# Optimization experiments

Hardware: AMD Instinct MI355X
Metric: run time of the kernel (lower is better)

The kernel has to match this reference:

```python
import jax, jax.numpy as jnp
import numpy as np
import math

BS, S, D = 2, 2048, 2048
DOWN, UP, H, RD = 512, 1024, 16, 32
HD = D // H            # 128, used only in softmax scale
VD = UP // H           # 64 per-head value dim
CD = UP // H           # 64 per-head content q/k dim
SCALE = math.sqrt(HD) + math.sqrt(RD)


def _rope(x, head_dim):
    # x: [bs, heads, seq, head_dim]; standard rotate-half RoPE
    seq = x.shape[2]
    inv_freq = 1.0 / (10000.0 ** (jnp.arange(0, head_dim, 2, dtype=jnp.float32) / head_dim))
    freqs = jnp.arange(seq, dtype=jnp.float32)[:, None] * inv_freq[None, :]  # [S, hd/2]
    emb = jnp.concatenate([freqs, freqs], axis=-1)                            # [S, hd]
    cos = jnp.cos(emb)[None, None]
    sin = jnp.sin(emb)[None, None]
    x1, x2 = x[..., : head_dim // 2], x[..., head_dim // 2 :]
    rot = jnp.concatenate([-x2, x1], axis=-1)
    return x * cos + rot * sin


def setup_inputs() -> dict:
    key = jax.random.key(0)
    ks = jax.random.split(key, 10)
    sd = 0.02
    inp = {
        'h': jax.random.normal(ks[0], (BS, S, D), jnp.float32),
        'mask': jnp.tril(jnp.ones((1, 1, S, S), jnp.int32)),
        'Wdkv': jax.random.normal(ks[1], (DOWN, D), jnp.float32) * sd,
        'bdkv': jnp.zeros((DOWN,), jnp.float32),
        'Wuk': jax.random.normal(ks[2], (UP, DOWN), jnp.float32) * sd,
        'buk': jnp.zeros((UP,), jnp.float32),
        'Wuv': jax.random.normal(ks[3], (UP, DOWN), jnp.float32) * sd,
        'buv': jnp.zeros((UP,), jnp.float32),
        'Wdq': jax.random.normal(ks[4], (DOWN, D), jnp.float32) * sd,
        'bdq': jnp.zeros((DOWN,), jnp.float32),
        'Wuq': jax.random.normal(ks[5], (UP, DOWN), jnp.float32) * sd,
        'buq': jnp.zeros((UP,), jnp.float32),
        'Wqr': jax.random.normal(ks[6], (RD * H, DOWN), jnp.float32) * sd,
        'bqr': jnp.zeros((RD * H,), jnp.float32),
        'Wkr': jax.random.normal(ks[7], (RD, D), jnp.float32) * sd,
        'bkr': jnp.zeros((RD,), jnp.float32),
        'Wfc': jax.random.normal(ks[8], (D, H * VD), jnp.float32) * sd,
        'bfc': jnp.zeros((D,), jnp.float32),
    }
    return inp


def reference(h, mask, Wdkv, bdkv, Wuk, buk, Wuv, buv, Wdq, bdq, Wuq, buq,
              Wqr, bqr, Wkr, bkr, Wfc, bfc):
    bs, seq, _ = h.shape
    # low-rank KV path
    c_kv = h @ Wdkv.T + bdkv                                   # [bs,S,DOWN]
    k_c = (c_kv @ Wuk.T + buk).reshape(bs, seq, H, CD).transpose(0, 2, 1, 3)
    v_c = (c_kv @ Wuv.T + buv).reshape(bs, seq, H, VD).transpose(0, 2, 1, 3)
    # low-rank Q path
    c_q = h @ Wdq.T + bdq                                      # [bs,S,DOWN]
    q_c = (c_q @ Wuq.T + buq).reshape(bs, seq, H, CD).transpose(0, 2, 1, 3)
    # decoupled RoPE paths
    q_r = _rope((c_q @ Wqr.T + bqr).reshape(bs, seq, H, RD).transpose(0, 2, 1, 3), RD)
    k_r = _rope((h @ Wkr.T + bkr).reshape(bs, seq, 1, RD).transpose(0, 2, 1, 3), RD)
    k_r = jnp.broadcast_to(k_r, (bs, H, seq, RD))              # shared RoPE key across heads
    q = jnp.concatenate([q_c, q_r], axis=-1)                   # [bs,H,S,CD+RD]
    k = jnp.concatenate([k_c, k_r], axis=-1)
    scores = jnp.einsum('bhqd,bhkd->bhqk', q, k)
    # NB: original applies mask BEFORE dividing by scale
    scores = jnp.where(mask == 0, -1e9, scores)
    probs = jax.nn.softmax(scores / SCALE, axis=-1)
    out = jnp.einsum('bhqk,bhkd->bhqd', probs, v_c)            # [bs,H,S,VD]
    out = out.transpose(0, 2, 1, 3).reshape(bs, seq, H * VD)
    return out @ Wfc.T + bfc
```

## Files before the change

kernel.cpp:

```cpp
#include <hip/hip_runtime.h>
#include <hip/hip_bf16.h>
#include <math.h>

typedef unsigned short u16;
typedef __attribute__((ext_vector_type(8))) short bf16x8;
typedef __attribute__((ext_vector_type(4))) float f32x4;
typedef __attribute__((ext_vector_type(16))) float f32x16;

namespace {

constexpr int BS = 2;
constexpr int S = 2048;
constexpr int D = 2048;
constexpr int DOWN = 512;
constexpr int UP = 1024;
constexpr int H = 16;
constexpr int RD = 32;
constexpr int VD = 64;
constexpr int QKD = 96;
constexpr int M = BS * S;
constexpr int N1 = 1152;
constexpr int N2 = 2048;
constexpr int N3 = 1536;
constexpr long PACK_V8 = (long)BS * H * S * QKD / 8;

__device__ __forceinline__ float b2f(u16 u) {
  unsigned int x = ((unsigned int)u) << 16;
  return __uint_as_float(x);
}
__device__ __forceinline__ u16 f2b(float f) {
  unsigned int u = __float_as_uint(f);
  u += 0x7fff + ((u >> 16) & 1);
  return (u16)(u >> 16);
}
__device__ __forceinline__ void store_out(float* p, float v) { *p = v; }
__device__ __forceinline__ void store_out(u16* p, float v) { *p = f2b(v); }

__device__ __forceinline__ void async16(const u16* g, u16* lds) {
  __builtin_amdgcn_global_load_lds(
      (const __attribute__((address_space(1))) unsigned int*)g,
      (__attribute__((address_space(3))) unsigned int*)lds, 16, 0, 0);
}

__device__ __forceinline__ float exp2_fast(float x) {
#if __has_builtin(__builtin_amdgcn_exp2f)
  return __builtin_amdgcn_exp2f(x);
#else
  float r;
  asm("v_exp_f32 %0, %1" : "=v"(r) : "v"(x));
  return r;
#endif
}

__device__ __forceinline__ unsigned pkbf(float a, float b) {
  union { __hip_bfloat162 h; unsigned u; } c;
  c.h = __float22bfloat162_rn(make_float2(a, b));
  return c.u;
}
__device__ __forceinline__ void plswap(unsigned& a, unsigned& b) {
  asm("v_permlane32_swap_b32 %0, %1" : "+v"(a), "+v"(b));
}

__device__ __forceinline__ f32x4 mfma32(bf16x8 a, bf16x8 b, f32x4 c) {
  return __builtin_amdgcn_mfma_f32_16x16x32_bf16(a, b, c, 0, 0, 0);
}
__device__ __forceinline__ f32x16 mfma3216(bf16x8 a, bf16x8 b, f32x16 c) {
  return __builtin_amdgcn_mfma_f32_32x32x16_bf16(a, b, c, 0, 0, 0);
}

__global__ __launch_bounds__(256) void prep_kernel(
    const float* __restrict__ h, const float* __restrict__ Wdkv,
    const float* __restrict__ Wdq, const float* __restrict__ Wkr,
    const float* __restrict__ Wuk, const float* __restrict__ Wuv,
    const float* __restrict__ Wuq, const float* __restrict__ Wqr,
    const float* __restrict__ Wfc, const float* __restrict__ bdkv,
    const float* __restrict__ bdq, const float* __restrict__ bkr,
    const float* __restrict__ buk, const float* __restrict__ buv,
    const float* __restrict__ buq, const float* __restrict__ bqr,
    u16* __restrict__ hb, u16* __restrict__ Wcat1, u16* __restrict__ Wcat2,
    u16* __restrict__ Wcat3, u16* __restrict__ Wfcb,
    float* __restrict__ bcat1, float* __restrict__ bcat2,
    float* __restrict__ bcat3, float* __restrict__ ct, float* __restrict__ st) {
  const long i = (long)blockIdx.x * 256 + threadIdx.x;
  if (i >= 3630240) return;
  if (i < 3620864) {
    const float* src; u16* dst; long off;
    if      (i < 2097152) { src = h;    dst = hb;              off = i; }
    else if (i < 2359296) { src = Wdkv; dst = Wcat1;           off = i - 2097152; }
    else if (i < 2621440) { src = Wdq;  dst = Wcat1 + 1048576; off = i - 2359296; }
    else if (i < 2637824) { src = Wkr;  dst = Wcat1 + 2097152; off = i - 2621440; }
    else if (i < 2768896) { src = Wuk;  dst = Wcat2;           off = i - 2637824; }
    else if (i < 2899968) { src = Wuv;  dst = Wcat2 + 524288;  off = i - 2768896; }
    else if (i < 3031040) { src = Wuq;  dst = Wcat3;           off = i - 2899968; }
    else if (i < 3096576) { src = Wqr;  dst = Wcat3 + 524288;  off = i - 3031040; }
    else                  { src = Wfc;  dst = Wfcb;            off = i - 3096576; }
    float4 v = ((const float4*)src)[off];
    ushort4 o;
    o.x = f2b(v.x); o.y = f2b(v.y); o.z = f2b(v.z); o.w = f2b(v.w);
    ((ushort4*)dst)[off] = o;
  } else if (i < 3622048) {
    long j0 = (i - 3620864) * 4;
#pragma unroll
    for (int e = 0; e < 4; ++e) {
      long j = j0 + e;
      if (j < N1) {
        float v = 0.f;
        if (j < 512) v = bdkv[j];
        else if (j < 1024) v = bdq[j - 512];
        else if (j < 1056) v = bkr[j - 1024];
        bcat1[j] = v;
      } else if (j < N1 + N2) {
        long jj = j - N1;
        bcat2[jj] = (jj < 1024) ? buk[jj] : buv[jj - 1024];
      } else {
        long jj = j - N1 - N2;
        bcat3[jj] = (jj < 1024) ? buq[jj] : bqr[jj - 1024];
      }
    }
  } else {
    long k0 = (i - 3622048) * 4;
#pragma unroll
    for (int e = 0; e < 4; ++e) {
      long k = k0 + e;
      int s = (int)(k >> 4), r = (int)(k & 15);
      float f = powf(10000.f, -(float)r / 16.f);
      float th = (float)s * f;
      ct[k] = cosf(th);
      st[k] = sinf(th);
    }
  }
}

template <int BM, int BN, typename OutT>
__device__ __forceinline__ void gemm_body(
    const u16* __restrict__ A, int lda, const u16* __restrict__ W, int ldw,
    const float* __restrict__ bias, OutT* __restrict__ C, int ldc, int K,
    int m0, int n0) {
  constexpr int MW = BM / 32;
  constexpr int NW = BN / 32;
  constexpr int AI = BM / 16;
  constexpr int TI = AI + BN / 16;
  __shared__ u16 As[2][BM * 32];
  __shared__ u16 Bs[2][BN * 32];
  const int t = threadIdx.x;
  const int lane = t & 63, wave = t >> 6;
  const int wm = (wave >> 1) * (BM / 2), wn = (wave & 1) * (BN / 2);
  const int lrow = lane & 15, lk = (lane >> 4) * 8;
  const int srow = lane >> 2, scol = (lane & 3) * 8;
  f32x4 acc[MW][NW] = {};

  auto stage = [&](int buf, int k0) {
    for (int i = wave; i < TI; i += 4) {
      if (i < AI) {
        int r = i * 16 + srow;
        async16(A + (size_t)(m0 + r) * lda + k0 + scol, &As[buf][i * 512]);
      } else {
        int r = (i - AI) * 16 + srow;
        async16(W + (size_t)(n0 + r) * ldw + k0 + scol,
                &Bs[buf][(i - AI) * 512]);
      }
    }
  };

  const int nt = K / 32;
  stage(0, 0);
  __syncthreads();
  for (int ti = 0; ti < nt; ++ti) {
    const int buf = ti & 1;
    if (ti + 1 < nt) stage(buf ^ 1, (ti + 1) * 32);
    bf16x8 af[MW], bfr[NW];
#pragma unroll
    for (int i = 0; i < MW; ++i)
      af[i] = *(const bf16x8*)(&As[buf][(wm + i * 16 + lrow) * 32 + lk]);
#pragma unroll
    for (int i = 0; i < NW; ++i)
      bfr[i] = *(const bf16x8*)(&Bs[buf][(wn + i * 16 + lrow) * 32 + lk]);
#pragma unroll
    for (int mi = 0; mi < MW; ++mi)
#pragma unroll
      for (int ni = 0; ni < NW; ++ni)
        acc[mi][ni] = mfma32(af[mi], bfr[ni], acc[mi][ni]);
    __syncthreads();
  }
#pragma unroll
  for (int mi = 0; mi < MW; ++mi)
#pragma unroll
    for (int ni = 0; ni < NW; ++ni)
#pragma unroll
      for (int r = 0; r < 4; ++r) {
        int m = m0 + wm + mi * 16 + (lane >> 4) * 4 + r;
        int n = n0 + wn + ni * 16 + lrow;
        store_out(C + (size_t)m * ldc + n, acc[mi][ni][r] + bias[n]);
      }
}

template <int BM, int BN, typename OutT>
__global__ __launch_bounds__(256) void gemm_bt_mfma(
    const u16* __restrict__ A, int lda, const u16* __restrict__ W, int ldw,
    const float* __restrict__ bias, OutT* __restrict__ C, int ldc, int K) {
  gemm_body<BM, BN, OutT>(A, lda, W, ldw, bias, C, ldc, K,
                          blockIdx.x * BM, blockIdx.y * BN);
}

__global__ __launch_bounds__(256) void gemm_up_fused(
    const u16* __restrict__ C1v, const u16* __restrict__ Wcat2,
    const u16* __restrict__ Wcat3, const float* __restrict__ bcat2,
    const float* __restrict__ bcat3, u16* __restrict__ C2,
    u16* __restrict__ C3) {
  const int by = blockIdx.y;
  const u16* A;
  const u16* W;
  const float* bias;
  u16* C;
  int ldc, n0;
  if (by < 16) {
    A = C1v; W = Wcat2; bias = bcat2; C = C2; ldc = N2; n0 = by * 128;
  } else {
    A = C1v + DOWN; W = Wcat3; bias = bcat3; C = C3; ldc = N3;
    n0 = (by - 16) * 128;
  }
  gemm_body<128, 128, u16>(A, N1, W, DOWN, bias, C, ldc, DOWN,
                           blockIdx.x * 128, n0);
}

__global__ __launch_bounds__(256) void reshape_kernel(
    const u16* __restrict__ qc, const u16* __restrict__ qr,
    const u16* __restrict__ kc,
    const u16* __restrict__ kr,
    const float* __restrict__ ct, const float* __restrict__ st,
    const u16* __restrict__ vin,
    u16* __restrict__ Qp, u16* __restrict__ Kp, u16* __restrict__ VtB) {
  const int bid = blockIdx.x;
  if (bid < 6144) {
    const long i = (long)bid * 256 + threadIdx.x;
    const int which = (i >= PACK_V8);
    const long j8 = which ? i - PACK_V8 : i;
    const int g = (int)(j8 % 12);
    const long row = j8 / 12;
    const int s = (int)(row & (S - 1));
    const int h = (int)((row >> 11) & 15);
    const int b = (int)(row >> 15);
    bf16x8 o;
    if (which == 0) {
      const float sc = 1.44269504088896f / (sqrtf(128.f) + sqrtf(32.f));
      if (g < 8) {
        bf16x8 v =
            *(const bf16x8*)(qc + (size_t)(b * S + s) * N3 + h * VD + g * 8);
#pragma unroll
        for (int e = 0; e < 8; ++e) o[e] = (short)f2b(b2f((u16)v[e]) * sc);
      } else {
        const int r0 = (g - 8) * 8;
        const u16* qrow = qr + (size_t)(b * S + s) * N3 + h * RD;
        bf16x8 x8 = *(const bf16x8*)(qrow + r0);
        bf16x8 xp8 = *(const bf16x8*)(qrow + (r0 ^ 16));
        const float* cb = ct + s * 16 + (r0 & 15);
        const float* sn = st + s * 16 + (r0 & 15);
        const float sg = (r0 < 16) ? -1.f : 1.f;
#pragma unroll
        for (int e = 0; e < 8; ++e) {
          float val = b2f((u16)x8[e]) * cb[e] + sg * b2f((u16)xp8[e]) * sn[e];
          o[e] = (short)f2b(val * sc);
        }
      }
      *(bf16x8*)(Qp + j8 * 8) = o;
    } else {
      if (g < 8) {
        o = *(const bf16x8*)(kc + (size_t)(b * S + s) * N2 + h * VD + g * 8);
      } else {
        const int r0 = (g - 8) * 8;
        const u16* krow = kr + (size_t)(b * S + s) * N1;
        bf16x8 x8 = *(const bf16x8*)(krow + r0);
        bf16x8 xp8 = *(const bf16x8*)(krow + (r0 ^ 16));
        const float* cb = ct + s * 16 + (r0 & 15);
        const float* sn = st + s * 16 + (r0 & 15);
        const float sg = (r0 < 16) ? -1.f : 1.f;
#pragma unroll
        for (int e = 0; e < 8; ++e) {
          float val = b2f((u16)x8[e]) * cb[e] + sg * b2f((u16)xp8[e]) * sn[e];
          o[e] = (short)f2b(val);
        }
      }
      *(bf16x8*)(Kp + j8 * 8) = o;
    }
  } else {
    __shared__ u16 tile[64][72];
    const int tb = bid - 6144;
    const int m0 = (tb & 63) * 64;
    const int h = tb >> 6;
    const int r = threadIdx.x >> 2, c0 = (threadIdx.x & 3) * 16;
    *(bf16x8*)(&tile[r][c0]) =
        *(const bf16x8*)(vin + (size_t)(m0 + r) * N2 + h * VD + c0);
    *(bf16x8*)(&tile[r][c0 + 8]) =
        *(const bf16x8*)(vin + (size_t)(m0 + r) * N2 + h * VD + c0 + 8);
    __syncthreads();
    bf16x8 o0, o1;
#pragma unroll
    for (int jj = 0; jj < 8; ++jj) {
      o0[jj] = (short)tile[c0 + jj][r];
      o1[jj] = (short)tile[c0 + 8 + jj][r];
    }
    const int b = m0 / S, sb = m0 % S;
    size_t dst = ((size_t)(b * H + h) * 64 + ((sb + c0) >> 5)) * 2048 +
                 (size_t)r * 32 + ((sb + c0) & 31);
    *(bf16x8*)(VtB + dst) = o0;
    *(bf16x8*)(VtB + dst + 8) = o1;
  }
}

__global__ __launch_bounds__(256, 3) void attn_mfma(
    const u16* __restrict__ Qp, const u16* __restrict__ Kp,
    const u16* __restrict__ Vt, u16* __restrict__ attnb) {
  const int t = threadIdx.x, wave = t >> 6, lane = t & 63;
  const int l31 = lane & 31, hw = lane >> 5;
  const int xcd = (int)(blockIdx.x & 7), sub = (int)(blockIdx.x >> 3);
  const int bh = xcd * 4 + (sub & 3);
  const int tile = 63 - (sub >> 2);
  const int b = bh >> 4, h = bh & 15;
  const int q0w = tile * 32;
  const size_t hbo = (size_t)bh * S;
  constexpr long KSTR = (long)4 * 32 * QKD;
  constexpr long VSTR = (long)4 * 2048;

  __shared__ float red[3][64][33];

  bf16x8 qf[6];
  {
    const u16* qrow = Qp + (hbo + q0w + l31) * QKD + hw * 8;
#pragma unroll
    for (int c = 0; c < 6; ++c) qf[c] = *(const bf16x8*)(qrow + c * 16);
  }
  const f32x16 ZERO16 = {0,0,0,0,0,0,0,0,0,0,0,0,0,0,0,0};
  f32x16 O0 = ZERO16, O1 = ZERO16;
  float lsum = 0.f;
  const int q_abs = q0w + l31;
  const u16* vptr = Vt + (size_t)bh * 64 * 2048 + l31 * 32 + 8 * hw +
                    (size_t)wave * 2048;
  const u16* kptr = Kp + (hbo + (size_t)(wave * 32 + l31)) * QKD + hw * 8;

  auto loadK = [&](bf16x8* kf) {
#pragma unroll
    for (int c = 0; c < 6; ++c) kf[c] = *(const bf16x8*)(kptr + c * 16);
  };
  auto loadV = [&](const u16* p, bf16x8* vf) {
    vf[0] = *(const bf16x8*)(p);
    vf[1] = *(const bf16x8*)(p + 16);
    vf[2] = *(const bf16x8*)(p + 1024);
    vf[3] = *(const bf16x8*)(p + 1040);
  };
  auto finish = [&](const f32x16& sa, const f32x16& sb, const bf16x8* vf,
                    int m) {
    float e[16];
    if (m == tile) {
      const int k0 = m * 32;
#pragma unroll
      for (int r = 0; r < 16; ++r) {
        int key_abs = k0 + (r & 3) + 8 * (r >> 2) + 4 * hw;
        float v = exp2_fast(sa[r] + sb[r]);
        e[r] = (key_abs <= q_abs) ? v : 0.f;
      }
    } else {
#pragma unroll
      for (int r = 0; r < 16; ++r) e[r] = exp2_fast(sa[r] + sb[r]);
    }
    {
      float p0 = (e[0] + e[1]) + (e[2] + e[3]);
      float p1 = (e[4] + e[5]) + (e[6] + e[7]);
      float p2 = (e[8] + e[9]) + (e[10] + e[11]);
      float p3 = (e[12] + e[13]) + (e[14] + e[15]);
      lsum += (p0 + p1) + (p2 + p3);
    }
    unsigned w0 = pkbf(e[0], e[1]),   w1 = pkbf(e[2], e[3]);
    unsigned w2 = pkbf(e[4], e[5]),   w3 = pkbf(e[6], e[7]);
    unsigned w4 = pkbf(e[8], e[9]),   w5 = pkbf(e[10], e[11]);
    unsigned w6 = pkbf(e[12], e[13]), w7 = pkbf(e[14], e[15]);
    plswap(w0, w2); plswap(w1, w3); plswap(w4, w6); plswap(w5, w7);
    union { unsigned u[4]; bf16x8 v; } ua, ub;
    ua.u[0] = w0; ua.u[1] = w1; ua.u[2] = w2; ua.u[3] = w3;
    ub.u[0] = w4; ub.u[1] = w5; ub.u[2] = w6; ub.u[3] = w7;
    __builtin_amdgcn_s_setprio(1);
    O0 = mfma3216(ua.v, vf[0], O0);
    O1 = mfma3216(ua.v, vf[2], O1);
    O0 = mfma3216(ub.v, vf[1], O0);
    O1 = mfma3216(ub.v, vf[3], O1);
    __builtin_amdgcn_s_setprio(0);
  };

  if (tile >= wave) {
    bf16x8 kf[6], vfE[4], vfO[4];
    loadK(kf);
    loadV(vptr, vfE);
    int m = wave;
    while (true) {
      {
        const bool pf = (m + 4 <= tile);
        if (pf) { vptr += VSTR; loadV(vptr, vfO); }
        __builtin_amdgcn_s_setprio(1);
        f32x16 sa = mfma3216(kf[0], qf[0], ZERO16);
        f32x16 sb = mfma3216(kf[1], qf[1], ZERO16);
        sa = mfma3216(kf[2], qf[2], sa);
        sb = mfma3216(kf[3], qf[3], sb);
        sa = mfma3216(kf[4], qf[4], sa);
        sb = mfma3216(kf[5], qf[5], sb);
        __builtin_amdgcn_s_setprio(0);
        if (pf) { kptr += KSTR; loadK(kf); }
        finish(sa, sb, vfE, m);
      }
      m += 4;
      if (m > tile) break;
      {
        const bool pf = (m + 4 <= tile);
        if (pf) { vptr += VSTR; loadV(vptr, vfE); }
        __builtin_amdgcn_s_setprio(1);
        f32x16 sa = mfma3216(kf[0], qf[0], ZERO16);
        f32x16 sb = mfma3216(kf[1], qf[1], ZERO16);
        sa = mfma3216(kf[2], qf[2], sa);
        sb = mfma3216(kf[3], qf[3], sb);
        sa = mfma3216(kf[4], qf[4], sa);
        sb = mfma3216(kf[5], qf[5], sb);
        __builtin_amdgcn_s_setprio(0);
        if (pf) { kptr += KSTR; loadK(kf); }
        finish(sa, sb, vfO, m);
      }
      m += 4;
      if (m > tile) break;
    }
  }

  if (wave > 0) {
#pragma unroll
    for (int r = 0; r < 16; ++r) {
      red[wave - 1][lane][r] = O0[r];
      red[wave - 1][lane][16 + r] = O1[r];
    }
    red[wave - 1][lane][32] = lsum;
  }
  __syncthreads();
  if (wave == 0) {
#pragma unroll
    for (int w = 0; w < 3; ++w) {
#pragma unroll
      for (int r = 0; r < 16; ++r) {
        O0[r] += red[w][lane][r];
        O1[r] += red[w][lane][16 + r];
      }
      lsum += red[w][lane][32];
    }
    float tot = lsum + __shfl_xor(lsum, 32);
    u16* ob = attnb + (size_t)b * S * UP + h * VD;
#pragma unroll
    for (int r = 0; r < 16; ++r) {
      int rowq = (r & 3) + 8 * (r >> 2) + 4 * hw;
      float linv = 1.f / __shfl(tot, rowq);
      size_t rowoff = (size_t)(q0w + rowq) * UP;
      ob[rowoff + l31] = f2b(O0[r] * linv);
      ob[rowoff + 32 + l31] = f2b(O1[r] * linv);
    }
  }
}

}

extern "C" void kernel_launch(void* const* d_in, const int* in_sizes, int n_in,
                              void* d_out, int out_size, void* d_ws, size_t ws_size,
                              hipStream_t stream) {
  const float* h    = (const float*)d_in[0];
  const float* Wdkv = (const float*)d_in[2];
  const float* bdkv = (const float*)d_in[3];
  const float* Wuk  = (const float*)d_in[4];
  const float* buk  = (const float*)d_in[5];
  const float* Wuv  = (const float*)d_in[6];
  const float* buv  = (const float*)d_in[7];
  const float* Wdq  = (const float*)d_in[8];
  const float* bdq  = (const float*)d_in[9];
  const float* Wuq  = (const float*)d_in[10];
  const float* buq  = (const float*)d_in[11];
  const float* Wqr  = (const float*)d_in[12];
  const float* bqr  = (const float*)d_in[13];
  const float* Wkr  = (const float*)d_in[14];
  const float* bkr  = (const float*)d_in[15];
  const float* Wfc  = (const float*)d_in[16];
  const float* bfc  = (const float*)d_in[17];
  float* out = (float*)d_out;

  u16* p = (u16*)d_ws;
  u16* hb    = p; p += (size_t)M * D;
  u16* Wcat1 = p; p += (size_t)N1 * D;
  u16* Wcat2 = p; p += (size_t)N2 * DOWN;
  u16* Wcat3 = p; p += (size_t)N3 * DOWN;
  u16* Wfcb  = p; p += (size_t)D * UP;
  u16* C1    = p; p += (size_t)M * N1;
  u16* C2    = p; p += (size_t)M * N2;
  u16* C3    = p; p += (size_t)M * N3;
  u16* Qp    = p; p += 6291456;
  u16* Kp    = p; p += 6291456;
  u16* Vt    = p; p += (size_t)UP * M;
  float* bcat1 = (float*)p; p += 2 * N1;
  float* bcat2 = (float*)p; p += 2 * N2;
  float* bcat3 = (float*)p; p += 2 * N3;
  float* ct = (float*)p; p += 2 * S * 16;
  float* st = (float*)p; p += 2 * S * 16;
  u16* attnb = C1;

  prep_kernel<<<dim3(14181), 256, 0, stream>>>(
      h, Wdkv, Wdq, Wkr, Wuk, Wuv, Wuq, Wqr, Wfc,
      bdkv, bdq, bkr, buk, buv, buq, bqr,
      hb, Wcat1, Wcat2, Wcat3, Wfcb, bcat1, bcat2, bcat3, ct, st);

  gemm_bt_mfma<64, 64, u16><<<dim3(M / 64, N1 / 64), 256, 0, stream>>>(
      hb, D, Wcat1, D, bcat1, C1, N1, D);
  gemm_up_fused<<<dim3(M / 128, 28), 256, 0, stream>>>(
      C1, Wcat2, Wcat3, bcat2, bcat3, C2, C3);

  reshape_kernel<<<dim3(7168), 256, 0, stream>>>(
      C3, C3 + UP, C2, C1 + 2 * DOWN, ct, st, C2 + UP, Qp, Kp, Vt);

  attn_mfma<<<dim3(2048), 256, 0, stream>>>(Qp, Kp, Vt, attnb);

  gemm_bt_mfma<64, 128, float><<<dim3(M / 64, D / 128), 256, 0, stream>>>(
      attnb, UP, Wfcb, UP, bfc, out, D, UP);
}
```

Baseline: 304.4 us.

## Fuse Q/K content packing into up-projection epilogue and fold softmax scale into weights

```diff
diff --git a/kernel.cpp b/kernel.cpp
--- a/kernel.cpp
+++ b/kernel.cpp
@@ -22,7 +22,7 @@
 constexpr int N1 = 1152;
 constexpr int N2 = 2048;
 constexpr int N3 = 1536;
-constexpr long PACK_V8 = (long)BS * H * S * QKD / 8;
+constexpr long ROPE_V8 = (long)BS * H * S * 4;
 
 __device__ __forceinline__ float b2f(u16 u) {
   unsigned int x = ((unsigned int)u) << 16;
@@ -83,20 +83,22 @@
     float* __restrict__ bcat3, float* __restrict__ ct, float* __restrict__ st) {
   const long i = (long)blockIdx.x * 256 + threadIdx.x;
   if (i >= 3630240) return;
+  const float SC = 1.44269504088896f / (sqrtf(128.f) + sqrtf(32.f));
   if (i < 3620864) {
-    const float* src; u16* dst; long off;
+    const float* src; u16* dst; long off; float scl = 1.f;
     if      (i < 2097152) { src = h;    dst = hb;              off = i; }
     else if (i < 2359296) { src = Wdkv; dst = Wcat1;           off = i - 2097152; }
     else if (i < 2621440) { src = Wdq;  dst = Wcat1 + 1048576; off = i - 2359296; }
     else if (i < 2637824) { src = Wkr;  dst = Wcat1 + 2097152; off = i - 2621440; }
     else if (i < 2768896) { src = Wuk;  dst = Wcat2;           off = i - 2637824; }
     else if (i < 2899968) { src = Wuv;  dst = Wcat2 + 524288;  off = i - 2768896; }
-    else if (i < 3031040) { src = Wuq;  dst = Wcat3;           off = i - 2899968; }
-    else if (i < 3096576) { src = Wqr;  dst = Wcat3 + 524288;  off = i - 3031040; }
+    else if (i < 3031040) { src = Wuq;  dst = Wcat3;           off = i - 2899968; scl = SC; }
+    else if (i < 3096576) { src = Wqr;  dst = Wcat3 + 524288;  off = i - 3031040; scl = SC; }
     else                  { src = Wfc;  dst = Wfcb;            off = i - 3096576; }
     float4 v = ((const float4*)src)[off];
     ushort4 o;
-    o.x = f2b(v.x); o.y = f2b(v.y); o.z = f2b(v.z); o.w = f2b(v.w);
+    o.x = f2b(v.x * scl); o.y = f2b(v.y * scl);
+    o.z = f2b(v.z * scl); o.w = f2b(v.w * scl);
     ((ushort4*)dst)[off] = o;
   } else if (i < 3622048) {
     long j0 = (i - 3620864) * 4;
@@ -114,7 +116,7 @@
         bcat2[jj] = (jj < 1024) ? buk[jj] : buv[jj - 1024];
       } else {
         long jj = j - N1 - N2;
-        bcat3[jj] = (jj < 1024) ? buq[jj] : bqr[jj - 1024];
+        bcat3[jj] = ((jj < 1024) ? buq[jj] : bqr[jj - 1024]) * SC;
       }
     }
   } else {
@@ -132,10 +134,63 @@
 }
 
 template <int BM, int BN, typename OutT>
-__device__ __forceinline__ void gemm_body(
+__device__ __forceinline__ void gemm_body_sb(
     const u16* __restrict__ A, int lda, const u16* __restrict__ W, int ldw,
     const float* __restrict__ bias, OutT* __restrict__ C, int ldc, int K,
     int m0, int n0) {
+  constexpr int MW = BM / 32;
+  constexpr int NW = BN / 32;
+  constexpr int AI = BM / 16;
+  constexpr int TI = AI + BN / 16;
+  __shared__ u16 As[BM * 32];
+  __shared__ u16 Bs[BN * 32];
+  const int t = threadIdx.x;
+  const int lane = t & 63, wave = t >> 6;
+  const int wm = (wave >> 1) * (BM / 2), wn = (wave & 1) * (BN / 2);
+  const int lrow = lane & 15, lk = (lane >> 4) * 8;
+  const int srow = lane >> 2, scol = (lane & 3) * 8;
+  f32x4 acc[MW][NW] = {};
+  for (int k0 = 0; k0 < K; k0 += 32) {
+    __syncthreads();
+    for (int i = wave; i < TI; i += 4) {
+      if (i < AI) {
+        int r = i * 16 + srow;
+        async16(A + (size_t)(m0 + r) * lda + k0 + scol, As + i * 512);
+      } else {
+        int r = (i - AI) * 16 + srow;
+        async16(W + (size_t)(n0 + r) * ldw + k0 + scol, Bs + (i - AI) * 512);
+      }
+    }
+    __syncthreads();
+    bf16x8 af[MW], bfr[NW];
+#pragma unroll
+    for (int i = 0; i < MW; ++i)
+      af[i] = *(const bf16x8*)(As + (wm + i * 16 + lrow) * 32 + lk);
+#pragma unroll
+    for (int i = 0; i < NW; ++i)
+      bfr[i] = *(const bf16x8*)(Bs + (wn + i * 16 + lrow) * 32 + lk);
+#pragma unroll
+    for (int mi = 0; mi < MW; ++mi)
+#pragma unroll
+      for (int ni = 0; ni < NW; ++ni)
+        acc[mi][ni] = mfma32(af[mi], bfr[ni], acc[mi][ni]);
+  }
+#pragma unroll
+  for (int mi = 0; mi < MW; ++mi)
+#pragma unroll
+    for (int ni = 0; ni < NW; ++ni)
+#pragma unroll
+      for (int r = 0; r < 4; ++r) {
+        int m = m0 + wm + mi * 16 + (lane >> 4) * 4 + r;
+        int n = n0 + wn + ni * 16 + lrow;
+        store_out(C + (size_t)m * ldc + n, acc[mi][ni][r] + bias[n]);
+      }
+}
+
+template <int BM, int BN, typename F>
+__device__ __forceinline__ void gemm_core_db(
+    const u16* __restrict__ A, int lda, const u16* __restrict__ W, int ldw,
+    const float* __restrict__ bias, int K, int m0, int n0, F&& emit) {
   constexpr int MW = BM / 32;
   constexpr int NW = BN / 32;
   constexpr int AI = BM / 16;
@@ -190,101 +245,104 @@
       for (int r = 0; r < 4; ++r) {
         int m = m0 + wm + mi * 16 + (lane >> 4) * 4 + r;
         int n = n0 + wn + ni * 16 + lrow;
-        store_out(C + (size_t)m * ldc + n, acc[mi][ni][r] + bias[n]);
+        emit(m, n, acc[mi][ni][r] + bias[n]);
       }
 }
 
 template <int BM, int BN, typename OutT>
-__global__ __launch_bounds__(256) void gemm_bt_mfma(
+__global__ __launch_bounds__(256) void gemm_bt_sb(
     const u16* __restrict__ A, int lda, const u16* __restrict__ W, int ldw,
     const float* __restrict__ bias, OutT* __restrict__ C, int ldc, int K) {
-  gemm_body<BM, BN, OutT>(A, lda, W, ldw, bias, C, ldc, K,
-                          blockIdx.x * BM, blockIdx.y * BN);
+  gemm_body_sb<BM, BN, OutT>(A, lda, W, ldw, bias, C, ldc, K,
+                             blockIdx.x * BM, blockIdx.y * BN);
+}
+
+template <int BM, int BN, typename OutT>
+__global__ __launch_bounds__(256) void gemm_bt_db(
+    const u16* __restrict__ A, int lda, const u16* __restrict__ W, int ldw,
+    const float* __restrict__ bias, OutT* __restrict__ C, int ldc, int K) {
+  gemm_core_db<BM, BN>(A, lda, W, ldw, bias, K, blockIdx.x * BM,
+                       blockIdx.y * BN, [&](int m, int n, float v) {
+                         store_out(C + (size_t)m * ldc + n, v);
+                       });
 }
 
 __global__ __launch_bounds__(256) void gemm_up_fused(
     const u16* __restrict__ C1v, const u16* __restrict__ Wcat2,
     const u16* __restrict__ Wcat3, const float* __restrict__ bcat2,
     const float* __restrict__ bcat3, u16* __restrict__ C2,
-    u16* __restrict__ C3) {
+    u16* __restrict__ C3, u16* __restrict__ Qp, u16* __restrict__ Kp) {
   const int by = blockIdx.y;
-  const u16* A;
-  const u16* W;
-  const float* bias;
-  u16* C;
-  int ldc, n0;
   if (by < 16) {
-    A = C1v; W = Wcat2; bias = bcat2; C = C2; ldc = N2; n0 = by * 128;
+    gemm_core_db<128, 128>(
+        C1v, N1, Wcat2, DOWN, bcat2, DOWN, blockIdx.x * 128, by * 128,
+        [&](int m, int n, float v) {
+          if (n < 1024) {
+            int b = m >> 11, s = m & 2047, hh = n >> 6, d = n & 63;
+            Kp[((size_t)(b * 16 + hh) * 2048 + s) * 96 + d] = f2b(v);
+          } else {
+            C2[(size_t)m * N2 + n] = f2b(v);
+          }
+        });
   } else {
-    A = C1v + DOWN; W = Wcat3; bias = bcat3; C = C3; ldc = N3;
-    n0 = (by - 16) * 128;
-  }
-  gemm_body<128, 128, u16>(A, N1, W, DOWN, bias, C, ldc, DOWN,
-                           blockIdx.x * 128, n0);
+    gemm_core_db<128, 128>(
+        C1v + DOWN, N1, Wcat3, DOWN, bcat3, DOWN, blockIdx.x * 128,
+        (by - 16) * 128, [&](int m, int n, float v) {
+          if (n < 1024) {
+            int b = m >> 11, s = m & 2047, hh = n >> 6, d = n & 63;
+            Qp[((size_t)(b * 16 + hh) * 2048 + s) * 96 + d] = f2b(v);
+          } else {
+            C3[(size_t)m * N3 + n] = f2b(v);
+          }
+        });
+  }
 }
 
 __global__ __launch_bounds__(256) void reshape_kernel(
-    const u16* __restrict__ qc, const u16* __restrict__ qr,
-    const u16* __restrict__ kc,
+    const u16* __restrict__ qr,
     const u16* __restrict__ kr,
     const float* __restrict__ ct, const float* __restrict__ st,
     const u16* __restrict__ vin,
     u16* __restrict__ Qp, u16* __restrict__ Kp, u16* __restrict__ VtB) {
   const int bid = blockIdx.x;
-  if (bid < 6144) {
+  if (bid < 2048) {
     const long i = (long)bid * 256 + threadIdx.x;
-    const int which = (i >= PACK_V8);
-    const long j8 = which ? i - PACK_V8 : i;
-    const int g = (int)(j8 % 12);
-    const long row = j8 / 12;
+    const int which = (i >= ROPE_V8);
+    const long j = which ? i - ROPE_V8 : i;
+    const int gg = (int)(j & 3);
+    const long row = j >> 2;
     const int s = (int)(row & (S - 1));
     const int h = (int)((row >> 11) & 15);
     const int b = (int)(row >> 15);
+    const int r0 = gg * 8;
+    const float* cb = ct + s * 16 + (r0 & 15);
+    const float* sn = st + s * 16 + (r0 & 15);
+    const float sg = (r0 < 16) ? -1.f : 1.f;
     bf16x8 o;
     if (which == 0) {
-      const float sc = 1.44269504088896f / (sqrtf(128.f) + sqrtf(32.f));
-      if (g < 8) {
-        bf16x8 v =
-            *(const bf16x8*)(qc + (size_t)(b * S + s) * N3 + h * VD + g * 8);
-#pragma unroll
-        for (int e = 0; e < 8; ++e) o[e] = (short)f2b(b2f((u16)v[e]) * sc);
-      } else {
-        const int r0 = (g - 8) * 8;
-        const u16* qrow = qr + (size_t)(b * S + s) * N3 + h * RD;
-        bf16x8 x8 = *(const bf16x8*)(qrow + r0);
-        bf16x8 xp8 = *(const bf16x8*)(qrow + (r0 ^ 16));
-        const float* cb = ct + s * 16 + (r0 & 15);
-        const float* sn = st + s * 16 + (r0 & 15);
-        const float sg = (r0 < 16) ? -1.f : 1.f;
-#pragma unroll
-        for (int e = 0; e < 8; ++e) {
-          float val = b2f((u16)x8[e]) * cb[e] + sg * b2f((u16)xp8[e]) * sn[e];
-          o[e] = (short)f2b(val * sc);
-        }
-      }
-      *(bf16x8*)(Qp + j8 * 8) = o;
+      const u16* qrow = qr + (size_t)(b * S + s) * N3 + h * RD;
+      bf16x8 x8 = *(const bf16x8*)(qrow + r0);
+      bf16x8 xp8 = *(const bf16x8*)(qrow + (r0 ^ 16));
+#pragma unroll
+      for (int e = 0; e < 8; ++e) {
+        float val = b2f((u16)x8[e]) * cb[e] + sg * b2f((u16)xp8[e]) * sn[e];
+        o[e] = (short)f2b(val);
+      }
+      *(bf16x8*)(Qp + row * 96 + 64 + r0) = o;
     } else {
-      if (g < 8) {
-        o = *(const bf16x8*)(kc + (size_t)(b * S + s) * N2 + h * VD + g * 8);
-      } else {
-        const int r0 = (g - 8) * 8;
-        const u16* krow = kr + (size_t)(b * S + s) * N1;
-        bf16x8 x8 = *(const bf16x8*)(krow + r0);
-        bf16x8 xp8 = *(const bf16x8*)(krow + (r0 ^ 16));
-        const float* cb = ct + s * 16 + (r0 & 15);
-        const float* sn = st + s * 16 + (r0 & 15);
-        const float sg = (r0 < 16) ? -1.f : 1.f;
-#pragma unroll
-        for (int e = 0; e < 8; ++e) {
-          float val = b2f((u16)x8[e]) * cb[e] + sg * b2f((u16)xp8[e]) * sn[e];
-          o[e] = (short)f2b(val);
-        }
-      }
-      *(bf16x8*)(Kp + j8 * 8) = o;
+      const u16* krow = kr + (size_t)(b * S + s) * N1;
+      bf16x8 x8 = *(const bf16x8*)(krow + r0);
+      bf16x8 xp8 = *(const bf16x8*)(krow + (r0 ^ 16));
+#pragma unroll
+      for (int e = 0; e < 8; ++e) {
+        float val = b2f((u16)x8[e]) * cb[e] + sg * b2f((u16)xp8[e]) * sn[e];
+        o[e] = (short)f2b(val);
+      }
+      *(bf16x8*)(Kp + row * 96 + 64 + r0) = o;
     }
   } else {
     __shared__ u16 tile[64][72];
-    const int tb = bid - 6144;
+    const int tb = bid - 2048;
     const int m0 = (tb & 63) * 64;
     const int h = tb >> 6;
     const int r = threadIdx.x >> 2, c0 = (threadIdx.x & 3) * 16;
@@ -506,16 +564,16 @@
       bdkv, bdq, bkr, buk, buv, buq, bqr,
       hb, Wcat1, Wcat2, Wcat3, Wfcb, bcat1, bcat2, bcat3, ct, st);
 
-  gemm_bt_mfma<64, 64, u16><<<dim3(M / 64, N1 / 64), 256, 0, stream>>>(
+  gemm_bt_sb<64, 64, u16><<<dim3(M / 64, N1 / 64), 256, 0, stream>>>(
       hb, D, Wcat1, D, bcat1, C1, N1, D);
   gemm_up_fused<<<dim3(M / 128, 28), 256, 0, stream>>>(
-      C1, Wcat2, Wcat3, bcat2, bcat3, C2, C3);
-
-  reshape_kernel<<<dim3(7168), 256, 0, stream>>>(
-      C3, C3 + UP, C2, C1 + 2 * DOWN, ct, st, C2 + UP, Qp, Kp, Vt);
+      C1, Wcat2, Wcat3, bcat2, bcat3, C2, C3, Qp, Kp);
+
+  reshape_kernel<<<dim3(3072), 256, 0, stream>>>(
+      C3 + UP, C1 + 2 * DOWN, ct, st, C2 + UP, Qp, Kp, Vt);
 
   attn_mfma<<<dim3(2048), 256, 0, stream>>>(Qp, Kp, Vt, attnb);
 
-  gemm_bt_mfma<64, 128, float><<<dim3(M / 64, D / 128), 256, 0, stream>>>(
+  gemm_bt_db<64, 128, float><<<dim3(M / 64, D / 128), 256, 0, stream>>>(
       attnb, UP, Wfcb, UP, bfc, out, D, UP);
 }
```

After: 306.4 us. Within noise of the previous version (+0.7%).
